# Optimization experiments

Hardware: AMD Instinct MI355X
Metric: run time of the kernel (lower is better)

The kernel has to match this reference:

```python
import jax, jax.numpy as jnp
import numpy as np

B, L, A = 16, 32, 2046
M = A + 2  # user col + attributors + item col = 2048 nodes


def _xavier_uniform(key, shape, gain):
    fan_out, fan_in = shape  # torch 2D param: fan_in = shape[1], fan_out = shape[0]
    bound = gain * np.sqrt(6.0 / (fan_in + fan_out))
    return jax.random.uniform(key, shape, jnp.float32, -bound, bound)


def setup_inputs() -> dict:
    key = jax.random.key(0)
    k = jax.random.split(key, 7)
    user = jax.random.normal(k[0], (B, 6 * L, 1), jnp.float32)
    item = jax.random.normal(k[1], (B, 6 * L, 1), jnp.float32)
    attributor = jax.random.normal(k[2], (B, 6 * L, A), jnp.float32)
    adj = (jax.random.uniform(k[3], (M, M)) < 0.5).astype(jnp.float32)
    initial_weight = jax.random.normal(k[4], (M, M), jnp.float32)
    W_1 = _xavier_uniform(k[5], (6 * L, A), gain=np.sqrt(2.0))  # relu gain
    W_2 = _xavier_uniform(k[6], (6 * L, L), gain=1.44)
    return {"user": user, "item": item, "attributor": attributor,
            "adj": adj, "initial_weight": initial_weight,
            "W_1": W_1, "W_2": W_2}


def reference(user, item, attributor, adj, initial_weight, W_1, W_2):
    N = W_2.shape[1]  # = length L
    a = attributor * W_1                                   # (B, 6L, A)
    raw = jnp.concatenate([user, a, item], axis=2)         # (B, 6L, M)
    Q, K, V = jnp.split(raw, 3, axis=1)                    # each (B, 2L, M)
    r = jax.nn.relu
    # (relu(X).T @ W).T  ==  einsum over the 2L dim -> (B, L, M)
    Query = jnp.einsum('bnm,nl->blm', r(Q), W_2[:2 * N])
    Key = jnp.einsum('bnm,nl->blm', r(K), W_2[2 * N:4 * N])
    Value = jnp.einsum('bnm,nl->blm', r(V), W_2[4 * N:])
    # h = Query.mT @ Key * adj * initial_weight  -> (B, M, M)
    h = jnp.einsum('blm,bln->bmn', Query, Key) * adj * initial_weight
    d = h - jnp.swapaxes(h, -1, -2)
    exp_h = jnp.exp(jnp.where(d > 0, 0.0, d))              # exp(min(d, 0))
    causal = exp_h / (exp_h + jnp.swapaxes(exp_h, -1, -2)) * adj  # (B, M, M)
    Ans = Value @ causal                                    # (B, L, M)
    idx = jnp.array([0, Ans.shape[2] - 1])
    return Ans[:, :, idx]                                   # (B, L, 2)
```

## Files before the change

kernel.cpp:

```cpp
#include <hip/hip_runtime.h>
#include <math.h>

#define BB 16
#define LL 32
#define AA 2046
#define MM 2048
#define NROWS 192


__device__ __forceinline__ size_t Pidx(int rc, int j, int b, int n) {
  return ((size_t)(rc * 2 + j) * BB + b) * MM + n;
}

__global__ __launch_bounds__(256) void prep_kernel(
    const float* __restrict__ user, const float* __restrict__ item,
    const float* __restrict__ W2, float* __restrict__ uv,
    float* __restrict__ part) {
  const int b = blockIdx.x, t = threadIdx.x;
  __shared__ float KQ[4][LL];
  __shared__ float uvs[4][64];
  if (t < 128) {
    const int q = t >> 5, l = t & 31;
    const float* __restrict__ src = (q == 0 || q == 2) ? user : item;
    const int rbase = (q < 2) ? 64 : 0;
    float acc = 0.f;
#pragma unroll
    for (int r = 0; r < 64; ++r)
      acc += fmaxf(src[b * NROWS + rbase + r], 0.f) * W2[(rbase + r) * LL + l];
    KQ[q][l] = acc;
  }
  __syncthreads();
  {
    const int which = t >> 6, r = t & 63;
    const int wrow = (which < 2) ? r : 64 + r;
    float acc = 0.f;
#pragma unroll
    for (int l = 0; l < LL; ++l) acc += W2[wrow * LL + l] * KQ[which][l];
    uvs[which][r] = acc;
    uv[which * (BB * 64) + b * 64 + r] = acc;
  }
  __syncthreads();
  if (t < 8) {
    const int nsel = t & 1, j = (t >> 1) & 1, z = t >> 2;
    const float* __restrict__ src = nsel ? item : user;
    float acc = 0.f;
#pragma unroll
    for (int i = 0; i < 64; ++i)
      acc += fmaxf(src[b * NROWS + z * 64 + i], 0.f) * uvs[2 * z + j][i];
    const int n = nsel ? (MM - 1) : 0;
    part[Pidx(2 * z, j, b, n)] = acc;
    part[Pidx(2 * z + 1, j, b, n)] = 0.f;
  }
}

__global__ __launch_bounds__(256) void st_kernel(
    const float* __restrict__ att, const float* __restrict__ W1,
    const float* __restrict__ uv, float* __restrict__ part) {
  const int col = blockIdx.x * 256 + threadIdx.x;
  const int b = blockIdx.y, rc = blockIdx.z;
  if (col >= AA) return;
  const int z = rc >> 1;
  const float* __restrict__ w0 = uv + (2 * z) * (BB * 64) + b * 64;
  const float* __restrict__ w1 = uv + (2 * z + 1) * (BB * 64) + b * 64;
  const int r0 = rc * 32;
  float a0 = 0.f, a1 = 0.f;
#pragma unroll
  for (int i = 0; i < 32; ++i) {
    const int r = r0 + i;
    const float v =
        fmaxf(att[(size_t)(b * NROWS + r) * AA + col] * W1[(size_t)r * AA + col],
              0.f);
    const int wi = r - z * 64;
    a0 += v * w0[wi];
    a1 += v * w1[wi];
  }
  const int n = col + 1;
  part[Pidx(rc, 0, b, n)] = a0;
  part[Pidx(rc, 1, b, n)] = a1;
}

__global__ __launch_bounds__(256) void cweight_kernel(
    const float* __restrict__ adj, const float* __restrict__ iw,
    const float* __restrict__ part, float* __restrict__ c) {
  const int idx = blockIdx.x * 256 + threadIdx.x;
  const int b = idx >> 11, n = idx & (MM - 1);
  const float s0 = part[Pidx(0, 0, b, n)] + part[Pidx(1, 0, b, n)];
  const float s1 = part[Pidx(0, 1, b, n)] + part[Pidx(1, 1, b, n)];
  const float t0 = part[Pidx(2, 0, b, n)] + part[Pidx(3, 0, b, n)];
  const float t1 = part[Pidx(2, 1, b, n)] + part[Pidx(3, 1, b, n)];
  const float an0 = adj[(size_t)n * MM];
  const float an1 = adj[(size_t)n * MM + (MM - 1)];
  const float wn0 = an0 * iw[(size_t)n * MM];
  const float wn1 = an1 * iw[(size_t)n * MM + (MM - 1)];
  const float w0n = adj[n] * iw[n];
  const float w1n =
      adj[(size_t)(MM - 1) * MM + n] * iw[(size_t)(MM - 1) * MM + n];
  const float d0 = s0 * wn0 - t0 * w0n;
  const float d1 = s1 * wn1 - t1 * w1n;
  const float e0 = expf(-fabsf(d0));
  const float e1 = expf(-fabsf(d1));
  const float sig0 = (d0 > 0.f) ? 1.f / (1.f + e0) : e0 / (1.f + e0);
  const float sig1 = (d1 > 0.f) ? 1.f / (1.f + e1) : e1 / (1.f + e1);
  c[b * MM + n] = sig0 * an0;
  c[BB * MM + b * MM + n] = sig1 * an1;
}

__global__ __launch_bounds__(256) void gather_kernel(
    const float* __restrict__ user, const float* __restrict__ item,
    const float* __restrict__ att, const float* __restrict__ W1,
    const float* __restrict__ c, const float* __restrict__ W2,
    float* __restrict__ out) {
  const int rv = blockIdx.x, b = blockIdx.y, tid = threadIdx.x;
  const int r = 128 + rv;
  const int gr = b * NROWS + r;
  const float* __restrict__ c0 = c + b * MM;
  const float* __restrict__ c1 = c + BB * MM + b * MM;
  float g0 = 0.f, g1 = 0.f;
#pragma unroll
  for (int i = 0; i < 8; ++i) {
    const int col = i * 256 + tid;
    if (col < AA) {
      const float v = fmaxf(
          att[(size_t)gr * AA + col] * W1[(size_t)r * AA + col], 0.f);
      g0 += v * c0[col + 1];
      g1 += v * c1[col + 1];
    }
  }
  if (tid == 0) {
    const float uval = fmaxf(user[gr], 0.f);
    const float ival = fmaxf(item[gr], 0.f);
    g0 += uval * c0[0] + ival * c0[MM - 1];
    g1 += uval * c1[0] + ival * c1[MM - 1];
  }
  __shared__ float r0[256], r1[256];
  r0[tid] = g0;
  r1[tid] = g1;
  __syncthreads();
  for (int s = 128; s > 0; s >>= 1) {
    if (tid < s) {
      r0[tid] += r0[tid + s];
      r1[tid] += r1[tid + s];
    }
    __syncthreads();
  }
  if (tid < 64) {
    const int l = tid & 31, j = tid >> 5;
    const float g = j ? r1[0] : r0[0];
    atomicAdd(&out[b * (LL * 2) + l * 2 + j], W2[r * LL + l] * g);
  }
}

extern "C" void kernel_launch(void* const* d_in, const int* in_sizes, int n_in,
                              void* d_out, int out_size, void* d_ws,
                              size_t ws_size, hipStream_t stream) {
  const float* user = (const float*)d_in[0];
  const float* item = (const float*)d_in[1];
  const float* att = (const float*)d_in[2];
  const float* adj = (const float*)d_in[3];
  const float* iw = (const float*)d_in[4];
  const float* W1 = (const float*)d_in[5];
  const float* W2 = (const float*)d_in[6];
  float* out = (float*)d_out;

  float* uv = (float*)d_ws;
  float* part = uv + 4 * BB * 64;
  float* c = part + 8 * BB * MM;

  hipMemsetAsync(d_out, 0, sizeof(float) * (size_t)out_size, stream);

  prep_kernel<<<dim3(BB), 256, 0, stream>>>(user, item, W2, uv, part);
  st_kernel<<<dim3(8, BB, 4), 256, 0, stream>>>(att, W1, uv, part);
  cweight_kernel<<<dim3(BB * MM / 256), 256, 0, stream>>>(adj, iw, part, c);
  gather_kernel<<<dim3(64, BB), 256, 0, stream>>>(user, item, att, W1, c, W2,
                                                  out);
}
```

Baseline: 113.0 us.

## Fuse all stages into one cooperative kernel with a grid-wide sync

Four kernels plus a memset are replaced by one cooperative kernel of 256 blocks. Each block computes its uv vectors locally, does the column-tile S/T reductions in shared memory, computes the causal weights c, then calls grid.sync before the gather stage. The gather stage stages c into LDS, processes four rows per block and reduces with wavefront shuffles instead of a shared-memory tree. This removes launch overhead and the global partial-sum round trips, at the cost of redundant prep work in every block and a grid-wide barrier.

```diff
diff --git a/kernel.cpp b/kernel.cpp
--- a/kernel.cpp
+++ b/kernel.cpp
@@ -1,5 +1,8 @@
 #include <hip/hip_runtime.h>
+#include <hip/hip_cooperative_groups.h>
 #include <math.h>
+
+namespace cg = cooperative_groups;
 
 #define BB 16
 #define LL 32
@@ -7,20 +10,28 @@
 #define MM 2048
 #define NROWS 192
 
-
-__device__ __forceinline__ size_t Pidx(int rc, int j, int b, int n) {
-  return ((size_t)(rc * 2 + j) * BB + b) * MM + n;
-}
-
-__global__ __launch_bounds__(256) void prep_kernel(
+#define NBLK 256
+#define NTHR 512
+
+
+__global__ __launch_bounds__(NTHR) void fused_kernel(
     const float* __restrict__ user, const float* __restrict__ item,
-    const float* __restrict__ W2, float* __restrict__ uv,
-    float* __restrict__ part) {
-  const int b = blockIdx.x, t = threadIdx.x;
+    const float* __restrict__ att, const float* __restrict__ adj,
+    const float* __restrict__ iw, const float* __restrict__ W1,
+    const float* __restrict__ W2, float* __restrict__ c,
+    float* __restrict__ out) {
+  cg::grid_group grid = cg::this_grid();
+  const int bid = blockIdx.x, tid = threadIdx.x;
+  const int b = bid >> 4, ctile = bid & 15;
+
   __shared__ float KQ[4][LL];
   __shared__ float uvs[4][64];
-  if (t < 128) {
-    const int q = t >> 5, l = t & 31;
+  __shared__ float stS[4][128][2];
+  __shared__ float cs0[MM], cs1[MM];
+  __shared__ float wred[8][4][2];
+
+  if (tid < 128) {
+    const int q = tid >> 5, l = tid & 31;
     const float* __restrict__ src = (q == 0 || q == 2) ? user : item;
     const int rbase = (q < 2) ? 64 : 0;
     float acc = 0.f;
@@ -30,123 +41,143 @@
     KQ[q][l] = acc;
   }
   __syncthreads();
-  {
-    const int which = t >> 6, r = t & 63;
+  if (tid < 256) {
+    const int which = tid >> 6, r = tid & 63;
     const int wrow = (which < 2) ? r : 64 + r;
     float acc = 0.f;
 #pragma unroll
     for (int l = 0; l < LL; ++l) acc += W2[wrow * LL + l] * KQ[which][l];
     uvs[which][r] = acc;
-    uv[which * (BB * 64) + b * 64 + r] = acc;
-  }
-  __syncthreads();
-  if (t < 8) {
-    const int nsel = t & 1, j = (t >> 1) & 1, z = t >> 2;
-    const float* __restrict__ src = nsel ? item : user;
-    float acc = 0.f;
-#pragma unroll
-    for (int i = 0; i < 64; ++i)
-      acc += fmaxf(src[b * NROWS + z * 64 + i], 0.f) * uvs[2 * z + j][i];
-    const int n = nsel ? (MM - 1) : 0;
-    part[Pidx(2 * z, j, b, n)] = acc;
-    part[Pidx(2 * z + 1, j, b, n)] = 0.f;
-  }
-}
-
-__global__ __launch_bounds__(256) void st_kernel(
-    const float* __restrict__ att, const float* __restrict__ W1,
-    const float* __restrict__ uv, float* __restrict__ part) {
-  const int col = blockIdx.x * 256 + threadIdx.x;
-  const int b = blockIdx.y, rc = blockIdx.z;
-  if (col >= AA) return;
-  const int z = rc >> 1;
-  const float* __restrict__ w0 = uv + (2 * z) * (BB * 64) + b * 64;
-  const float* __restrict__ w1 = uv + (2 * z + 1) * (BB * 64) + b * 64;
-  const int r0 = rc * 32;
-  float a0 = 0.f, a1 = 0.f;
-#pragma unroll
-  for (int i = 0; i < 32; ++i) {
-    const int r = r0 + i;
-    const float v =
-        fmaxf(att[(size_t)(b * NROWS + r) * AA + col] * W1[(size_t)r * AA + col],
-              0.f);
-    const int wi = r - z * 64;
-    a0 += v * w0[wi];
-    a1 += v * w1[wi];
-  }
-  const int n = col + 1;
-  part[Pidx(rc, 0, b, n)] = a0;
-  part[Pidx(rc, 1, b, n)] = a1;
-}
-
-__global__ __launch_bounds__(256) void cweight_kernel(
-    const float* __restrict__ adj, const float* __restrict__ iw,
-    const float* __restrict__ part, float* __restrict__ c) {
-  const int idx = blockIdx.x * 256 + threadIdx.x;
-  const int b = idx >> 11, n = idx & (MM - 1);
-  const float s0 = part[Pidx(0, 0, b, n)] + part[Pidx(1, 0, b, n)];
-  const float s1 = part[Pidx(0, 1, b, n)] + part[Pidx(1, 1, b, n)];
-  const float t0 = part[Pidx(2, 0, b, n)] + part[Pidx(3, 0, b, n)];
-  const float t1 = part[Pidx(2, 1, b, n)] + part[Pidx(3, 1, b, n)];
-  const float an0 = adj[(size_t)n * MM];
-  const float an1 = adj[(size_t)n * MM + (MM - 1)];
-  const float wn0 = an0 * iw[(size_t)n * MM];
-  const float wn1 = an1 * iw[(size_t)n * MM + (MM - 1)];
-  const float w0n = adj[n] * iw[n];
-  const float w1n =
-      adj[(size_t)(MM - 1) * MM + n] * iw[(size_t)(MM - 1) * MM + n];
-  const float d0 = s0 * wn0 - t0 * w0n;
-  const float d1 = s1 * wn1 - t1 * w1n;
-  const float e0 = expf(-fabsf(d0));
-  const float e1 = expf(-fabsf(d1));
-  const float sig0 = (d0 > 0.f) ? 1.f / (1.f + e0) : e0 / (1.f + e0);
-  const float sig1 = (d1 > 0.f) ? 1.f / (1.f + e1) : e1 / (1.f + e1);
-  c[b * MM + n] = sig0 * an0;
-  c[BB * MM + b * MM + n] = sig1 * an1;
-}
-
-__global__ __launch_bounds__(256) void gather_kernel(
-    const float* __restrict__ user, const float* __restrict__ item,
-    const float* __restrict__ att, const float* __restrict__ W1,
-    const float* __restrict__ c, const float* __restrict__ W2,
-    float* __restrict__ out) {
-  const int rv = blockIdx.x, b = blockIdx.y, tid = threadIdx.x;
-  const int r = 128 + rv;
-  const int gr = b * NROWS + r;
-  const float* __restrict__ c0 = c + b * MM;
-  const float* __restrict__ c1 = c + BB * MM + b * MM;
-  float g0 = 0.f, g1 = 0.f;
-#pragma unroll
-  for (int i = 0; i < 8; ++i) {
-    const int col = i * 256 + tid;
+  }
+  __syncthreads();
+
+  {
+    const int colidx = tid & 127, q = tid >> 7;
+    const int col = ctile * 128 + colidx;
+    const int r0 = q * 32;
+    const float* __restrict__ wj0 = uvs[(q < 2) ? 0 : 2];
+    const float* __restrict__ wj1 = uvs[(q < 2) ? 1 : 3];
+    const int wbase = (q < 2) ? 0 : 64;
+    float a0 = 0.f, a1 = 0.f;
     if (col < AA) {
-      const float v = fmaxf(
-          att[(size_t)gr * AA + col] * W1[(size_t)r * AA + col], 0.f);
-      g0 += v * c0[col + 1];
-      g1 += v * c1[col + 1];
-    }
-  }
-  if (tid == 0) {
-    const float uval = fmaxf(user[gr], 0.f);
-    const float ival = fmaxf(item[gr], 0.f);
-    g0 += uval * c0[0] + ival * c0[MM - 1];
-    g1 += uval * c1[0] + ival * c1[MM - 1];
-  }
-  __shared__ float r0[256], r1[256];
-  r0[tid] = g0;
-  r1[tid] = g1;
-  __syncthreads();
-  for (int s = 128; s > 0; s >>= 1) {
-    if (tid < s) {
-      r0[tid] += r0[tid + s];
-      r1[tid] += r1[tid + s];
-    }
-    __syncthreads();
-  }
+#pragma unroll
+      for (int i = 0; i < 32; ++i) {
+        const int r = r0 + i;
+        const float v = fmaxf(
+            att[((size_t)(b * NROWS + r)) * AA + col] * W1[(size_t)r * AA + col],
+            0.f);
+        a0 += v * wj0[r - wbase];
+        a1 += v * wj1[r - wbase];
+      }
+    } else {
+      const float* __restrict__ src = (col == AA) ? user : item;
+#pragma unroll
+      for (int i = 0; i < 32; ++i) {
+        const int r = r0 + i;
+        const float v = fmaxf(src[b * NROWS + r], 0.f);
+        a0 += v * wj0[r - wbase];
+        a1 += v * wj1[r - wbase];
+      }
+    }
+    stS[q][colidx][0] = a0;
+    stS[q][colidx][1] = a1;
+  }
+  __syncthreads();
+
+  if (tid < 128) {
+    const int i = tid;
+    const int cc = ctile * 128 + i;
+    const int n = (cc < AA) ? cc + 1 : ((cc == AA) ? 0 : MM - 1);
+    const float s0 = stS[0][i][0] + stS[1][i][0];
+    const float s1 = stS[0][i][1] + stS[1][i][1];
+    const float t0 = stS[2][i][0] + stS[3][i][0];
+    const float t1 = stS[2][i][1] + stS[3][i][1];
+    const float an0 = adj[(size_t)n * MM];
+    const float an1 = adj[(size_t)n * MM + (MM - 1)];
+    const float wn0 = an0 * iw[(size_t)n * MM];
+    const float wn1 = an1 * iw[(size_t)n * MM + (MM - 1)];
+    const float w0n = adj[n] * iw[n];
+    const float w1n =
+        adj[(size_t)(MM - 1) * MM + n] * iw[(size_t)(MM - 1) * MM + n];
+    const float d0 = s0 * wn0 - t0 * w0n;
+    const float d1 = s1 * wn1 - t1 * w1n;
+    const float e0 = expf(-fabsf(d0));
+    const float e1 = expf(-fabsf(d1));
+    const float sig0 = (d0 > 0.f) ? 1.f / (1.f + e0) : e0 / (1.f + e0);
+    const float sig1 = (d1 > 0.f) ? 1.f / (1.f + e1) : e1 / (1.f + e1);
+    __hip_atomic_store(&c[b * MM + n], sig0 * an0, __ATOMIC_RELAXED,
+                       __HIP_MEMORY_SCOPE_AGENT);
+    __hip_atomic_store(&c[BB * MM + b * MM + n], sig1 * an1, __ATOMIC_RELAXED,
+                       __HIP_MEMORY_SCOPE_AGENT);
+  }
+
+  if (bid == 0) {
+    __hip_atomic_store(&out[tid], 0.f, __ATOMIC_RELAXED,
+                       __HIP_MEMORY_SCOPE_AGENT);
+    __hip_atomic_store(&out[tid + NTHR], 0.f, __ATOMIC_RELAXED,
+                       __HIP_MEMORY_SCOPE_AGENT);
+  }
+
+  grid.sync();
+
+  const int gb = bid >> 4, rvt = bid & 15;
+#pragma unroll
+  for (int k = 0; k < 4; ++k) {
+    const int idx = k * NTHR + tid;
+    cs0[idx] = __hip_atomic_load(&c[gb * MM + idx], __ATOMIC_RELAXED,
+                                 __HIP_MEMORY_SCOPE_AGENT);
+    cs1[idx] = __hip_atomic_load(&c[BB * MM + gb * MM + idx], __ATOMIC_RELAXED,
+                                 __HIP_MEMORY_SCOPE_AGENT);
+  }
+  __syncthreads();
+
+#pragma unroll
+  for (int k = 0; k < 4; ++k) {
+    const int r = 128 + rvt * 4 + k;
+    float g0 = 0.f, g1 = 0.f;
+#pragma unroll
+    for (int ch = 0; ch < 4; ++ch) {
+      const int cl = ch * NTHR + tid;
+      if (cl < AA) {
+        const float v = fmaxf(att[((size_t)(gb * NROWS + r)) * AA + cl] *
+                                  W1[(size_t)r * AA + cl],
+                              0.f);
+        g0 += v * cs0[cl + 1];
+        g1 += v * cs1[cl + 1];
+      }
+    }
+    if (tid == NTHR - 2) {
+      const float v = fmaxf(user[gb * NROWS + r], 0.f);
+      g0 += v * cs0[0];
+      g1 += v * cs1[0];
+    }
+    if (tid == NTHR - 1) {
+      const float v = fmaxf(item[gb * NROWS + r], 0.f);
+      g0 += v * cs0[MM - 1];
+      g1 += v * cs1[MM - 1];
+    }
+#pragma unroll
+    for (int s = 32; s >= 1; s >>= 1) {
+      g0 += __shfl_xor(g0, s, 64);
+      g1 += __shfl_xor(g1, s, 64);
+    }
+    if ((tid & 63) == 0) {
+      wred[tid >> 6][k][0] = g0;
+      wred[tid >> 6][k][1] = g1;
+    }
+  }
+  __syncthreads();
   if (tid < 64) {
     const int l = tid & 31, j = tid >> 5;
-    const float g = j ? r1[0] : r0[0];
-    atomicAdd(&out[b * (LL * 2) + l * 2 + j], W2[r * LL + l] * g);
+    float acc = 0.f;
+#pragma unroll
+    for (int k = 0; k < 4; ++k) {
+      float gk = 0.f;
+#pragma unroll
+      for (int w = 0; w < 8; ++w) gk += wred[w][k][j];
+      acc += W2[(128 + rvt * 4 + k) * LL + l] * gk;
+    }
+    atomicAdd(&out[gb * (LL * 2) + l * 2 + j], acc);
   }
 }
 
@@ -161,16 +192,11 @@
   const float* W1 = (const float*)d_in[5];
   const float* W2 = (const float*)d_in[6];
   float* out = (float*)d_out;
-
-  float* uv = (float*)d_ws;
-  float* part = uv + 4 * BB * 64;
-  float* c = part + 8 * BB * MM;
-
-  hipMemsetAsync(d_out, 0, sizeof(float) * (size_t)out_size, stream);
-
-  prep_kernel<<<dim3(BB), 256, 0, stream>>>(user, item, W2, uv, part);
-  st_kernel<<<dim3(8, BB, 4), 256, 0, stream>>>(att, W1, uv, part);
-  cweight_kernel<<<dim3(BB * MM / 256), 256, 0, stream>>>(adj, iw, part, c);
-  gather_kernel<<<dim3(64, BB), 256, 0, stream>>>(user, item, att, W1, c, W2,
-                                                  out);
+  float* c = (float*)d_ws;
+
+  void* args[] = {(void*)&user, (void*)&item, (void*)&att,
+                  (void*)&adj,  (void*)&iw,   (void*)&W1,
+                  (void*)&W2,   (void*)&c,    (void*)&out};
+  hipLaunchCooperativeKernel((const void*)fused_kernel, dim3(NBLK), dim3(NTHR),
+                             args, 0, stream);
 }
```

Result: slower. 152.7 us (+35.2%).
